# Optimization experiments

Measured on AMD Instinct MI355X. Metric: run time of the kernel, lower is better.

The kernel has to match this reference:

```python
import jax, jax.numpy as jnp
import numpy as np

E = 512
H = 8
D = E // H  # head_dim = 64
SCALE = D ** -0.5
NEG_INF = float('-inf')


def layer_norm(x, g, b, eps=1e-5):
    mu = jnp.mean(x, axis=-1, keepdims=True)
    var = jnp.var(x, axis=-1, keepdims=True)
    return (x - mu) * jax.lax.rsqrt(var + eps) * g + b


def setup_inputs() -> dict:
    key = jax.random.key(0)
    ks = jax.random.split(key, 16)
    B, Q, K = 4, 2048, 2048
    inp = {
        'query': jax.random.normal(ks[0], (B, Q, E), jnp.float32),
        'key_value': jax.random.normal(ks[1], (B, K, E), jnp.float32),
        'kv_mask': jax.random.randint(ks[2], (B, K), 0, 2) > 0,
        'sparse_mask': jax.random.randint(ks[3], (B, Q, K), 0, 2) > 0,
        'ln_q_g': jnp.ones((E,), jnp.float32),
        'ln_q_b': jnp.zeros((E,), jnp.float32),
        'ln_kv_g': jnp.ones((E,), jnp.float32),
        'ln_kv_b': jnp.zeros((E,), jnp.float32),
        # Linear weights stored as (in, out): y = x @ W + b
        'Wq': jax.random.normal(ks[4], (E, E), jnp.float32) * (E ** -0.5),
        'bq': jnp.zeros((E,), jnp.float32),
        'Wk': jax.random.normal(ks[5], (E, E), jnp.float32) * (E ** -0.5),
        'bk': jnp.zeros((E,), jnp.float32),
        'Wv': jax.random.normal(ks[6], (E, E), jnp.float32) * (E ** -0.5),
        'bv': jnp.zeros((E,), jnp.float32),
        'Wo': jax.random.normal(ks[7], (E, E), jnp.float32) * (E ** -0.5),
        'bo': jnp.zeros((E,), jnp.float32),
    }
    return inp


def reference(query, key_value, kv_mask, sparse_mask,
              ln_q_g, ln_q_b, ln_kv_g, ln_kv_b,
              Wq, bq, Wk, bk, Wv, bv, Wo, bo):
    B, Qn, _ = query.shape
    Kn = key_value.shape[1]
    qn = layer_norm(query, ln_q_g, ln_q_b)
    kvn = layer_norm(key_value, ln_kv_g, ln_kv_b)
    q = (qn @ Wq + bq).reshape(B, Qn, H, D)
    k = (kvn @ Wk + bk).reshape(B, Kn, H, D)
    v = (kvn @ Wv + bv).reshape(B, Kn, H, D)
    # scores: [B, H, Q, K]
    scores = jnp.einsum('bqhd,bkhd->bhqk', q, k) * SCALE
    mask = kv_mask[:, None, None, :] & sparse_mask[:, None, :, :]
    scores = jnp.where(mask, scores, NEG_INF)
    attn = jax.nn.softmax(scores, axis=-1)
    # nan_to_num(0): rows with no valid key -> all-zero weights
    valid_row = jnp.any(mask, axis=-1, keepdims=True)
    attn = jnp.where(valid_row, attn, 0.0)
    out = jnp.einsum('bhqk,bkhd->bqhd', attn, v).reshape(B, Qn, E)
    return out @ Wo + bo
```

## Files before the change

### kernel.cpp

```cpp
#include <hip/hip_runtime.h>
#include <hip/hip_bf16.h>
#include <math.h>

typedef unsigned short ushort_t;
typedef __attribute__((ext_vector_type(8))) __bf16 bf16x8;
typedef __attribute__((ext_vector_type(4))) float f32x4;
typedef __attribute__((ext_vector_type(16))) float f32x16;
typedef __attribute__((ext_vector_type(4))) unsigned int u32x4;

#define E_DIM 512
#define HEADS 8
#define HD 64
#define SEQ 2048
#define NROWS 8192
#define NEGF (-1e30f)
#define QSCALE 0.18033688011112042f

static __device__ __forceinline__ unsigned short f2b(float f) {
  unsigned int x;
  __builtin_memcpy(&x, &f, 4);
  x += 0x7fffu + ((x >> 16) & 1u);
  return (unsigned short)(x >> 16);
}

static __device__ __forceinline__ unsigned cvt_pk_bf16(float lo, float hi) {
  unsigned r;
  asm("v_cvt_pk_bf16_f32 %0, %1, %2" : "=v"(r) : "v"(lo), "v"(hi));
  return r;
}

static __device__ __forceinline__ float fexp2(float x) {
  float r;
  asm("v_exp_f32 %0, %1" : "=v"(r) : "v"(x));
  return r;
}

static __device__ __forceinline__ int swz(int row, int col) {
  return row * 64 + ((((col >> 3) ^ (row & 7)) & 7) << 3) + (col & 7);
}

static __device__ __forceinline__ void gl2lds16(const ushort_t* g, ushort_t* s) {
#if __has_builtin(__builtin_amdgcn_global_load_lds)
  __builtin_amdgcn_global_load_lds(
      (const __attribute__((address_space(1))) unsigned int*)(uintptr_t)g,
      (__attribute__((address_space(3))) unsigned int*)(uintptr_t)s,
      16, 0, 0);
#else
  int l = threadIdx.x & 63;
  *(u32x4*)(s + l * 8) = *(const u32x4*)g;
#endif
}

__launch_bounds__(256)
__global__ void prep_kernel(const float* __restrict__ Wq, const float* __restrict__ Wk,
                            const float* __restrict__ Wv, const float* __restrict__ Wo,
                            ushort_t* __restrict__ WT,
                            const int* __restrict__ kvm, const int* __restrict__ sp,
                            unsigned long long* __restrict__ bits,
                            const float* __restrict__ xq, const float* __restrict__ xkv,
                            const float* __restrict__ gq, const float* __restrict__ bq,
                            const float* __restrict__ gkv, const float* __restrict__ bkv,
                            ushort_t* __restrict__ yq, ushort_t* __restrict__ ykv) {
  int blk = blockIdx.x;
  int t = threadIdx.x;
  if (blk < 1024) {
    int z = blk >> 8, rem = blk & 255;
    const float* in = (z == 0) ? Wq : (z == 1) ? Wk : (z == 2) ? Wv : Wo;
    ushort_t* o = WT + (size_t)z * E_DIM * E_DIM;
    __shared__ float tile[32 * 33];
    int tx = t & 31, ty = t >> 5;
    int n0 = (rem & 15) * 32, k0 = (rem >> 4) * 32;
#pragma unroll
    for (int i = 0; i < 4; ++i) {
      int k = ty + i * 8;
      tile[k * 33 + tx] = in[(k0 + k) * E_DIM + n0 + tx];
    }
    __syncthreads();
#pragma unroll
    for (int i = 0; i < 4; ++i) {
      int n = ty + i * 8;
      o[(n0 + n) * E_DIM + k0 + tx] = f2b(tile[tx * 33 + n]);
    }
  } else if (blk < 3072) {
    int w = t >> 6, l = t & 63;
    int row = (blk - 1024) * 4 + w;
    int b = row >> 11;
    const int* sprow = sp + ((size_t)row << 11);
    const int* kvrow = kvm + (b << 11);
    unsigned long long* out = bits + ((size_t)row << 5);
#pragma unroll 4
    for (int it = 0; it < 32; ++it) {
      int k = it * 64 + l;
      unsigned long long m = __ballot(sprow[k] != 0 && kvrow[k] != 0);
      if (l == 0) out[it] = m;
    }
  } else {
    int idx = blk - 3072;
    int which = idx >> 11;
    const float* x = which ? xkv : xq;
    const float* g = which ? gkv : gq;
    const float* bb = which ? bkv : bq;
    ushort_t* y = which ? ykv : yq;
    int w = t >> 6, l = t & 63;
    int row = (idx & 2047) * 4 + w;
    f32x4 x0 = *(const f32x4*)&x[row * E_DIM + l * 8];
    f32x4 x1 = *(const f32x4*)&x[row * E_DIM + l * 8 + 4];
    float xf[8], s = 0.f, ss = 0.f;
#pragma unroll
    for (int j = 0; j < 8; ++j) {
      xf[j] = (j < 4) ? x0[j] : x1[j - 4];
      s += xf[j];
      ss += xf[j] * xf[j];
    }
#pragma unroll
    for (int off = 32; off > 0; off >>= 1) {
      s += __shfl_xor(s, off);
      ss += __shfl_xor(ss, off);
    }
    float mu = s * (1.f / 512.f);
    float var = fmaxf(ss * (1.f / 512.f) - mu * mu, 0.f);
    float rs = rsqrtf(var + 1e-5f);
    f32x4 g0 = *(const f32x4*)&g[l * 8];
    f32x4 g1 = *(const f32x4*)&g[l * 8 + 4];
    f32x4 b0 = *(const f32x4*)&bb[l * 8];
    f32x4 b1 = *(const f32x4*)&bb[l * 8 + 4];
#pragma unroll
    for (int j = 0; j < 8; ++j) {
      float gv = (j < 4) ? g0[j] : g1[j - 4];
      float bv = (j < 4) ? b0[j] : b1[j - 4];
      y[row * E_DIM + l * 8 + j] = f2b((xf[j] - mu) * rs * gv + bv);
    }
  }
}

template <int MODE>
static __device__ __forceinline__ void gemm_core64(ushort_t* lA, ushort_t* lB,
                                                   const ushort_t* __restrict__ A,
                                                   const ushort_t* __restrict__ WT,
                                                   const float* __restrict__ bias,
                                                   void* Cv, float scale, int m0, int n0) {
  int t = threadIdx.x, w = t >> 6, l = t & 63;
  int quad = l >> 4, l15 = l & 15;
  int wm_ = w >> 1, wn_ = w & 1;
  int csrc = ((l & 7) ^ (l >> 3)) * 8;
  int rln = l >> 3;

  f32x4 acc[4][2] = {};
  for (int kk = 0; kk < E_DIM; kk += 64) {
    __syncthreads();
#pragma unroll
    for (int i = 0; i < 4; ++i) {
      int r0 = i * 32 + w * 8;
      gl2lds16(&A[(size_t)(m0 + r0 + rln) * E_DIM + kk + csrc], &lA[r0 * 64]);
    }
#pragma unroll
    for (int i = 0; i < 2; ++i) {
      int r0 = i * 32 + w * 8;
      gl2lds16(&WT[(size_t)(n0 + r0 + rln) * E_DIM + kk + csrc], &lB[r0 * 64]);
    }
    __syncthreads();
#pragma unroll
    for (int ks = 0; ks < 2; ++ks) {
      bf16x8 af[4], bf[2];
#pragma unroll
      for (int mt = 0; mt < 4; ++mt)
        af[mt] = *(const bf16x8*)&lA[swz(wm_ * 64 + mt * 16 + l15, ks * 32 + quad * 8)];
#pragma unroll
      for (int nt = 0; nt < 2; ++nt)
        bf[nt] = *(const bf16x8*)&lB[swz(wn_ * 32 + nt * 16 + l15, ks * 32 + quad * 8)];
#pragma unroll
      for (int mt = 0; mt < 4; ++mt)
#pragma unroll
        for (int nt = 0; nt < 2; ++nt)
          acc[mt][nt] = __builtin_amdgcn_mfma_f32_16x16x32_bf16(af[mt], bf[nt], acc[mt][nt], 0, 0, 0);
    }
  }

#pragma unroll
  for (int nt = 0; nt < 2; ++nt) {
    int col = n0 + wn_ * 32 + nt * 16 + l15;
    float bv = bias[col];
    if constexpr (MODE == 2) {
      int h = col >> 6, d = col & 63;
#pragma unroll
      for (int mt = 0; mt < 4; ++mt) {
        int row = m0 + wm_ * 64 + mt * 16 + quad * 4;
        int b = row >> 11, k = row & 2047;
        union { ushort_t u[4]; uint2 v; } pk;
#pragma unroll
        for (int r = 0; r < 4; ++r) pk.u[r] = f2b(acc[mt][nt][r] + bv);
        *(uint2*)&((ushort_t*)Cv)[((((size_t)(b * HEADS + h)) * HD + d) << 11) + k] = pk.v;
      }
    } else {
#pragma unroll
      for (int mt = 0; mt < 4; ++mt) {
#pragma unroll
        for (int r = 0; r < 4; ++r) {
          int rowm = m0 + wm_ * 64 + mt * 16 + quad * 4 + r;
          float val = (acc[mt][nt][r] + bv) * scale;
          if constexpr (MODE == 0)
            ((ushort_t*)Cv)[rowm * E_DIM + col] = f2b(val);
          else
            ((float*)Cv)[rowm * E_DIM + col] = val;
        }
      }
    }
  }
}

__launch_bounds__(256)
__global__ void proj3_kernel(const ushort_t* __restrict__ qn, const ushort_t* __restrict__ WTq,
                             const float* __restrict__ bq, ushort_t* __restrict__ qp,
                             const ushort_t* __restrict__ kvn, const ushort_t* __restrict__ WTv,
                             const float* __restrict__ bv, ushort_t* __restrict__ Vt,
                             const ushort_t* __restrict__ WTk, const float* __restrict__ bk,
                             ushort_t* __restrict__ kp, int zbase) {
  __shared__ ushort_t lA[128 * 64];
  __shared__ ushort_t lB[64 * 64];
  int flat = blockIdx.x;
  int chunk = gridDim.x >> 3;
  int work = (flat & 7) * chunk + (flat >> 3);
  int z = zbase + (work >> 9);
  int r = work & 511;
  int m0 = (r >> 3) * 128, n0 = (r & 7) * 64;
  if (z == 0)      gemm_core64<0>(lA, lB, qn,  WTq, bq, qp, QSCALE, m0, n0);
  else if (z == 1) gemm_core64<2>(lA, lB, kvn, WTv, bv, Vt, 1.f,    m0, n0);
  else             gemm_core64<0>(lA, lB, kvn, WTk, bk, kp, 1.f,    m0, n0);
}

__launch_bounds__(256)
__global__ void out_kernel(const ushort_t* __restrict__ A, const ushort_t* __restrict__ WT,
                           const float* __restrict__ bias, float* __restrict__ C) {
  __shared__ ushort_t lA[128 * 64];
  __shared__ ushort_t lB[64 * 64];
  int flat = blockIdx.x;
  int work = (flat & 7) * 64 + (flat >> 3);
  int m0 = (work >> 3) * 128, n0 = (work & 7) * 64;
  gemm_core64<1>(lA, lB, A, WT, bias, C, 1.f, m0, n0);
}

__launch_bounds__(256)
__global__ void attn_kernel(const ushort_t* __restrict__ Qp, const ushort_t* __restrict__ Kp,
                            const ushort_t* __restrict__ Vt,
                            const unsigned long long* __restrict__ bits,
                            ushort_t* __restrict__ ctx) {
  __shared__ __align__(16) char smemb[40960];
  ushort_t* sQ = (ushort_t*)smemb;
  int t = threadIdx.x, w = t >> 6, l = t & 63;
  int qw = w & 1, ks = w >> 1;
  ushort_t* sK = (ushort_t*)(smemb + 8192 + ks * 8192);
  ushort_t* sV = (ushort_t*)(smemb + 24576 + ks * 8192);
  int l31 = l & 31, half = l >> 5;

  int flat = blockIdx.x;
  int work = (flat & 7) * 128 + (flat >> 3);
  int qblk = work & 31;
  int h = (work >> 5) & 7;
  int b = work >> 8;
  int q0 = qblk * 64;
  int bh = b * HEADS + h;
  int myq = qw * 32 + l31;
  int csrc = ((l & 7) ^ (l >> 3)) * 8;
  int rln = l >> 3;

#pragma unroll
  for (int it = 0; it < 2; ++it) {
    int r0 = w * 16 + it * 8;
    gl2lds16(&Qp[(size_t)(b * SEQ + q0 + r0 + rln) * E_DIM + h * HD + csrc], &sQ[r0 * 64]);
  }

  const unsigned long long* mrow = bits + ((size_t)(b * SEQ + q0 + myq) << 5);
  float ls0 = 0.f, ls1 = 0.f, ls2 = 0.f, ls3 = 0.f;
  f32x16 o0 = {}, o1 = {};
  bf16x8 qf[4];

  for (int t16 = 0; t16 < 16; ++t16) {
    int kt = t16 * 2 + ks;
    int k0 = kt * 64;
    unsigned long long wmask = mrow[kt];
    __syncthreads();
#pragma unroll
    for (int it = 0; it < 4; ++it) {
      int r0 = (it * 2 + qw) * 8;
      gl2lds16(&Kp[(size_t)(b * SEQ + k0 + r0 + rln) * E_DIM + h * HD + csrc], &sK[r0 * 64]);
      gl2lds16(&Vt[((size_t)bh * HD + r0 + rln) * SEQ + k0 + csrc], &sV[r0 * 64]);
    }
    __syncthreads();
    if (t16 == 0) {
#pragma unroll
      for (int ds = 0; ds < 4; ++ds)
        qf[ds] = *(const bf16x8*)&sQ[swz(myq, ds * 16 + 8 * half)];
    }

    f32x16 s0 = {}, s1 = {};
    __builtin_amdgcn_s_setprio(1);
#pragma unroll
    for (int ds = 0; ds < 4; ++ds) {
      bf16x8 kf0 = *(const bf16x8*)&sK[swz(l31, ds * 16 + 8 * half)];
      bf16x8 kf1 = *(const bf16x8*)&sK[swz(32 + l31, ds * 16 + 8 * half)];
      s0 = __builtin_amdgcn_mfma_f32_32x32x16_bf16(kf0, qf[ds], s0, 0, 0, 0);
      s1 = __builtin_amdgcn_mfma_f32_32x32x16_bf16(kf1, qf[ds], s1, 0, 0, 0);
    }
    __builtin_amdgcn_s_setprio(0);

    bf16x8 pf[4];
#pragma unroll
    for (int kt2 = 0; kt2 < 2; ++kt2) {
      const f32x16& sv = kt2 ? s1 : s0;
      unsigned h32 = ((unsigned)(wmask >> (32 * kt2))) >> (4 * half);
      unsigned wa[4], wb[4];
#pragma unroll
      for (int g = 0; g < 4; ++g) {
        unsigned gb = h32 >> (8 * g);
        float p0 = fexp2((gb & 1u)        ? sv[g * 4 + 0] : NEGF);
        float p1 = fexp2(((gb >> 1) & 1u) ? sv[g * 4 + 1] : NEGF);
        float p2 = fexp2(((gb >> 2) & 1u) ? sv[g * 4 + 2] : NEGF);
        float p3 = fexp2(((gb >> 3) & 1u) ? sv[g * 4 + 3] : NEGF);
        ls0 += p0; ls1 += p1; ls2 += p2; ls3 += p3;
        wa[g] = cvt_pk_bf16(p0, p1);
        wb[g] = cvt_pk_bf16(p2, p3);
      }
      asm("v_permlane32_swap_b32 %0, %1" : "+v"(wa[0]), "+v"(wa[1]));
      asm("v_permlane32_swap_b32 %0, %1" : "+v"(wb[0]), "+v"(wb[1]));
      asm("v_permlane32_swap_b32 %0, %1" : "+v"(wa[2]), "+v"(wa[3]));
      asm("v_permlane32_swap_b32 %0, %1" : "+v"(wb[2]), "+v"(wb[3]));
      union { unsigned u[4]; bf16x8 v; } f0, f1;
      f0.u[0] = wa[0]; f0.u[1] = wb[0]; f0.u[2] = wa[1]; f0.u[3] = wb[1];
      f1.u[0] = wa[2]; f1.u[1] = wb[2]; f1.u[2] = wa[3]; f1.u[3] = wb[3];
      pf[kt2 * 2 + 0] = f0.v;
      pf[kt2 * 2 + 1] = f1.v;
    }

    __builtin_amdgcn_s_setprio(1);
#pragma unroll
    for (int ksp = 0; ksp < 4; ++ksp) {
      bf16x8 vf0 = *(const bf16x8*)&sV[swz(l31, ksp * 16 + 8 * half)];
      bf16x8 vf1 = *(const bf16x8*)&sV[swz(32 + l31, ksp * 16 + 8 * half)];
      o0 = __builtin_amdgcn_mfma_f32_32x32x16_bf16(vf0, pf[ksp], o0, 0, 0, 0);
      o1 = __builtin_amdgcn_mfma_f32_32x32x16_bf16(vf1, pf[ksp], o1, 0, 0, 0);
    }
    __builtin_amdgcn_s_setprio(0);
  }

  float lsum = (ls0 + ls1) + (ls2 + ls3);
  lsum += __shfl_xor(lsum, 32);

  __syncthreads();
  float* mrg = (float*)(smemb + 8192);
  if (ks == 1) {
    float* e = mrg + (qw * 64 + l) * 33;
#pragma unroll
    for (int r = 0; r < 16; ++r) e[r] = o0[r];
#pragma unroll
    for (int r = 0; r < 16; ++r) e[16 + r] = o1[r];
    e[32] = lsum;
  }
  __syncthreads();
  if (ks == 0) {
    const float* e = mrg + (qw * 64 + l) * 33;
#pragma unroll
    for (int r = 0; r < 16; ++r) o0[r] += e[r];
#pragma unroll
    for (int r = 0; r < 16; ++r) o1[r] += e[16 + r];
    lsum += e[32];
    float inv = (lsum > 0.f) ? 1.f / lsum : 0.f;
    size_t base = (size_t)(b * SEQ + q0 + myq) * E_DIM + h * HD;
#pragma unroll
    for (int dt = 0; dt < 2; ++dt) {
      const f32x16& oo = dt ? o1 : o0;
#pragma unroll
      for (int g = 0; g < 4; ++g) {
        union { ushort_t u[4]; uint2 v; } ov;
#pragma unroll
        for (int r = 0; r < 4; ++r) ov.u[r] = f2b(oo[g * 4 + r] * inv);
        *(uint2*)&ctx[base + dt * 32 + g * 8 + 4 * half] = ov.v;
      }
    }
  }
}

extern "C" void kernel_launch(void* const* d_in, const int* in_sizes, int n_in,
                              void* d_out, int out_size, void* d_ws, size_t ws_size,
                              hipStream_t stream) {
  const float* query     = (const float*)d_in[0];
  const float* key_value = (const float*)d_in[1];
  const int*   kv_mask   = (const int*)d_in[2];
  const int*   sp_mask   = (const int*)d_in[3];
  const float* ln_q_g  = (const float*)d_in[4];
  const float* ln_q_b  = (const float*)d_in[5];
  const float* ln_kv_g = (const float*)d_in[6];
  const float* ln_kv_b = (const float*)d_in[7];
  const float* Wq = (const float*)d_in[8];
  const float* bq = (const float*)d_in[9];
  const float* Wk = (const float*)d_in[10];
  const float* bk = (const float*)d_in[11];
  const float* Wv = (const float*)d_in[12];
  const float* bv = (const float*)d_in[13];
  const float* Wo = (const float*)d_in[14];
  const float* bo = (const float*)d_in[15];

  const size_t NB = (size_t)NROWS * E_DIM;
  char* ws = (char*)d_ws;
  ushort_t* bufA = (ushort_t*)ws;
  ushort_t* bufB = bufA + NB;
  ushort_t* WT   = bufB + NB;
  ushort_t* WTq = WT;
  ushort_t* WTk = WTq + E_DIM * E_DIM;
  ushort_t* WTv = WTk + E_DIM * E_DIM;
  ushort_t* WTo = WTv + E_DIM * E_DIM;
  unsigned long long* bits = (unsigned long long*)(WTo + E_DIM * E_DIM);
  ushort_t* bufC = (ushort_t*)(ws + (20u << 20));

  ushort_t* dlo = (ushort_t*)d_out;
  ushort_t* dhi = dlo + NB;

  bool fused = ws_size >= (28u << 20);
  ushort_t* kp = fused ? bufC : dlo;

  prep_kernel<<<7168, 256, 0, stream>>>(Wq, Wk, Wv, Wo, WT, kv_mask, sp_mask, bits,
                                        query, key_value, ln_q_g, ln_q_b, ln_kv_g, ln_kv_b,
                                        dlo, bufA);

  if (fused) {
    proj3_kernel<<<1536, 256, 0, stream>>>(dlo, WTq, bq, dhi,
                                           bufA, WTv, bv, bufB,
                                           WTk, bk, bufC, 0);
  } else {
    proj3_kernel<<<1024, 256, 0, stream>>>(dlo, WTq, bq, dhi,
                                           bufA, WTv, bv, bufB,
                                           WTk, bk, dlo, 0);
    proj3_kernel<<<512, 256, 0, stream>>>(dlo, WTq, bq, dhi,
                                          bufA, WTv, bv, bufB,
                                          WTk, bk, dlo, 2);
  }

  attn_kernel<<<1024, 256, 0, stream>>>(dhi, kp, bufB, bits, bufA);

  out_kernel<<<512, 256, 0, stream>>>(bufA, WTo, bo, (float*)d_out);
}
```

Before: 259.6 us.

## Use 128x128 projection tiles and MFMA-based softmax row sums with bitmask masking

The QKV projection now uses 128x128 output tiles per block, half the blocks of before, with a schedule that groups the Q/K/V column blocks per row tile, so each A tile is loaded fewer times. In attention, masking is done by ANDing the exp result with a sign-extended mask bit instead of selecting before exp. The row sum is computed by an extra MFMA against a ones vector instead of scalar adds and a shuffle. This adds accumulator registers (16 acc tiles in the GEMM, an extra f32x16 in attention), which may lower occupancy.

Result: no change. 264.8 us (+2.0%).

```diff
diff --git a/kernel.cpp b/kernel.cpp
--- a/kernel.cpp
+++ b/kernel.cpp
@@ -33,6 +33,14 @@
   float r;
   asm("v_exp_f32 %0, %1" : "=v"(r) : "v"(x));
   return r;
+}
+
+static __device__ __forceinline__ unsigned bitmask1(unsigned v, int off) {
+#if __has_builtin(__builtin_amdgcn_sbfe)
+  return (unsigned)__builtin_amdgcn_sbfe((int)v, off, 1);
+#else
+  return (unsigned)((int)(v << (31 - off)) >> 31);
+#endif
 }
 
 static __device__ __forceinline__ int swz(int row, int col) {
@@ -134,6 +142,77 @@
 }
 
 template <int MODE>
+static __device__ __forceinline__ void gemm_core128(ushort_t* lA, ushort_t* lB,
+                                                    const ushort_t* __restrict__ A,
+                                                    const ushort_t* __restrict__ WT,
+                                                    const float* __restrict__ bias,
+                                                    void* Cv, float scale, int m0, int n0) {
+  int t = threadIdx.x, w = t >> 6, l = t & 63;
+  int quad = l >> 4, l15 = l & 15;
+  int wm_ = w >> 1, wn_ = w & 1;
+  int csrc = ((l & 7) ^ (l >> 3)) * 8;
+  int rln = l >> 3;
+
+  f32x4 acc[4][4] = {};
+  for (int kk = 0; kk < E_DIM; kk += 64) {
+    __syncthreads();
+#pragma unroll
+    for (int i = 0; i < 4; ++i) {
+      int r0 = i * 32 + w * 8;
+      gl2lds16(&A[(size_t)(m0 + r0 + rln) * E_DIM + kk + csrc], &lA[r0 * 64]);
+      gl2lds16(&WT[(size_t)(n0 + r0 + rln) * E_DIM + kk + csrc], &lB[r0 * 64]);
+    }
+    __syncthreads();
+#pragma unroll
+    for (int ks = 0; ks < 2; ++ks) {
+      bf16x8 af[4], bf[4];
+#pragma unroll
+      for (int mt = 0; mt < 4; ++mt)
+        af[mt] = *(const bf16x8*)&lA[swz(wm_ * 64 + mt * 16 + l15, ks * 32 + quad * 8)];
+#pragma unroll
+      for (int nt = 0; nt < 4; ++nt)
+        bf[nt] = *(const bf16x8*)&lB[swz(wn_ * 64 + nt * 16 + l15, ks * 32 + quad * 8)];
+#pragma unroll
+      for (int mt = 0; mt < 4; ++mt)
+#pragma unroll
+        for (int nt = 0; nt < 4; ++nt)
+          acc[mt][nt] = __builtin_amdgcn_mfma_f32_16x16x32_bf16(af[mt], bf[nt], acc[mt][nt], 0, 0, 0);
+    }
+  }
+
+#pragma unroll
+  for (int nt = 0; nt < 4; ++nt) {
+    int col = n0 + wn_ * 64 + nt * 16 + l15;
+    float bv = bias[col];
+    if constexpr (MODE == 2) {
+      int h = col >> 6, d = col & 63;
+#pragma unroll
+      for (int mt = 0; mt < 4; ++mt) {
+        int row = m0 + wm_ * 64 + mt * 16 + quad * 4;
+        int b = row >> 11, k = row & 2047;
+        union { ushort_t u[4]; uint2 v; } pk;
+#pragma unroll
+        for (int r = 0; r < 4; ++r) pk.u[r] = f2b(acc[mt][nt][r] + bv);
+        *(uint2*)&((ushort_t*)Cv)[((((size_t)(b * HEADS + h)) * HD + d) << 11) + k] = pk.v;
+      }
+    } else {
+#pragma unroll
+      for (int mt = 0; mt < 4; ++mt) {
+#pragma unroll
+        for (int r = 0; r < 4; ++r) {
+          int rowm = m0 + wm_ * 64 + mt * 16 + quad * 4 + r;
+          float val = (acc[mt][nt][r] + bv) * scale;
+          if constexpr (MODE == 0)
+            ((ushort_t*)Cv)[rowm * E_DIM + col] = f2b(val);
+          else
+            ((float*)Cv)[rowm * E_DIM + col] = val;
+        }
+      }
+    }
+  }
+}
+
+template <int MODE>
 static __device__ __forceinline__ void gemm_core64(ushort_t* lA, ushort_t* lB,
                                                    const ushort_t* __restrict__ A,
                                                    const ushort_t* __restrict__ WT,
@@ -180,52 +259,47 @@
   for (int nt = 0; nt < 2; ++nt) {
     int col = n0 + wn_ * 32 + nt * 16 + l15;
     float bv = bias[col];
-    if constexpr (MODE == 2) {
-      int h = col >> 6, d = col & 63;
-#pragma unroll
-      for (int mt = 0; mt < 4; ++mt) {
-        int row = m0 + wm_ * 64 + mt * 16 + quad * 4;
-        int b = row >> 11, k = row & 2047;
-        union { ushort_t u[4]; uint2 v; } pk;
-#pragma unroll
-        for (int r = 0; r < 4; ++r) pk.u[r] = f2b(acc[mt][nt][r] + bv);
-        *(uint2*)&((ushort_t*)Cv)[((((size_t)(b * HEADS + h)) * HD + d) << 11) + k] = pk.v;
+#pragma unroll
+    for (int mt = 0; mt < 4; ++mt) {
+#pragma unroll
+      for (int r = 0; r < 4; ++r) {
+        int rowm = m0 + wm_ * 64 + mt * 16 + quad * 4 + r;
+        float val = (acc[mt][nt][r] + bv) * scale;
+        if constexpr (MODE == 0)
+          ((ushort_t*)Cv)[rowm * E_DIM + col] = f2b(val);
+        else
+          ((float*)Cv)[rowm * E_DIM + col] = val;
       }
-    } else {
-#pragma unroll
-      for (int mt = 0; mt < 4; ++mt) {
-#pragma unroll
-        for (int r = 0; r < 4; ++r) {
-          int rowm = m0 + wm_ * 64 + mt * 16 + quad * 4 + r;
-          float val = (acc[mt][nt][r] + bv) * scale;
-          if constexpr (MODE == 0)
-            ((ushort_t*)Cv)[rowm * E_DIM + col] = f2b(val);
-          else
-            ((float*)Cv)[rowm * E_DIM + col] = val;
-        }
-      }
-    }
-  }
-}
-
+    }
+  }
+}
+
+template <int SCHED>
 __launch_bounds__(256)
-__global__ void proj3_kernel(const ushort_t* __restrict__ qn, const ushort_t* __restrict__ WTq,
-                             const float* __restrict__ bq, ushort_t* __restrict__ qp,
-                             const ushort_t* __restrict__ kvn, const ushort_t* __restrict__ WTv,
-                             const float* __restrict__ bv, ushort_t* __restrict__ Vt,
-                             const ushort_t* __restrict__ WTk, const float* __restrict__ bk,
-                             ushort_t* __restrict__ kp, int zbase) {
+__global__ void proj_kernel(const ushort_t* __restrict__ qn, const ushort_t* __restrict__ WTq,
+                            const float* __restrict__ bq, ushort_t* __restrict__ qp,
+                            const ushort_t* __restrict__ kvn, const ushort_t* __restrict__ WTk,
+                            const float* __restrict__ bk, ushort_t* __restrict__ kp,
+                            const ushort_t* __restrict__ WTv, const float* __restrict__ bv,
+                            ushort_t* __restrict__ Vt) {
   __shared__ ushort_t lA[128 * 64];
-  __shared__ ushort_t lB[64 * 64];
+  __shared__ ushort_t lB[128 * 64];
+  constexpr int NBN = (SCHED == 0) ? 12 : (SCHED == 1) ? 8 : 4;
   int flat = blockIdx.x;
   int chunk = gridDim.x >> 3;
   int work = (flat & 7) * chunk + (flat >> 3);
-  int z = zbase + (work >> 9);
-  int r = work & 511;
-  int m0 = (r >> 3) * 128, n0 = (r & 7) * 64;
-  if (z == 0)      gemm_core64<0>(lA, lB, qn,  WTq, bq, qp, QSCALE, m0, n0);
-  else if (z == 1) gemm_core64<2>(lA, lB, kvn, WTv, bv, Vt, 1.f,    m0, n0);
-  else             gemm_core64<0>(lA, lB, kvn, WTk, bk, kp, 1.f,    m0, n0);
+  int nb = work % NBN;
+  int m0 = (work / NBN) * 128;
+  if constexpr (SCHED == 0) {
+    if (nb < 4)      gemm_core128<0>(lA, lB, qn,  WTq, bq, qp, QSCALE, m0, nb * 128);
+    else if (nb < 8) gemm_core128<0>(lA, lB, kvn, WTk, bk, kp, 1.f,    m0, (nb - 4) * 128);
+    else             gemm_core128<2>(lA, lB, kvn, WTv, bv, Vt, 1.f,    m0, (nb - 8) * 128);
+  } else if constexpr (SCHED == 1) {
+    if (nb < 4)      gemm_core128<0>(lA, lB, qn,  WTq, bq, qp, QSCALE, m0, nb * 128);
+    else             gemm_core128<2>(lA, lB, kvn, WTv, bv, Vt, 1.f,    m0, (nb - 4) * 128);
+  } else {
+    gemm_core128<0>(lA, lB, kvn, WTk, bk, kp, 1.f, m0, nb * 128);
+  }
 }
 
 __launch_bounds__(256)
@@ -270,9 +344,11 @@
   }
 
   const unsigned long long* mrow = bits + ((size_t)(b * SEQ + q0 + myq) << 5);
-  float ls0 = 0.f, ls1 = 0.f, ls2 = 0.f, ls3 = 0.f;
-  f32x16 o0 = {}, o1 = {};
+  f32x16 o0 = {}, o1 = {}, lacc = {};
   bf16x8 qf[4];
+  union { unsigned u[4]; bf16x8 v; } onec;
+#pragma unroll
+  for (int i = 0; i < 4; ++i) onec.u[i] = 0x3f803f80u;
 
   for (int t16 = 0; t16 < 16; ++t16) {
     int kt = t16 * 2 + ks;
@@ -311,14 +387,12 @@
       unsigned wa[4], wb[4];
 #pragma unroll
       for (int g = 0; g < 4; ++g) {
-        unsigned gb = h32 >> (8 * g);
-        float p0 = fexp2((gb & 1u)        ? sv[g * 4 + 0] : NEGF);
-        float p1 = fexp2(((gb >> 1) & 1u) ? sv[g * 4 + 1] : NEGF);
-        float p2 = fexp2(((gb >> 2) & 1u) ? sv[g * 4 + 2] : NEGF);
-        float p3 = fexp2(((gb >> 3) & 1u) ? sv[g * 4 + 3] : NEGF);
-        ls0 += p0; ls1 += p1; ls2 += p2; ls3 += p3;
-        wa[g] = cvt_pk_bf16(p0, p1);
-        wb[g] = cvt_pk_bf16(p2, p3);
+        unsigned q0u = __float_as_uint(fexp2(sv[g * 4 + 0])) & bitmask1(h32, 8 * g + 0);
+        unsigned q1u = __float_as_uint(fexp2(sv[g * 4 + 1])) & bitmask1(h32, 8 * g + 1);
+        unsigned q2u = __float_as_uint(fexp2(sv[g * 4 + 2])) & bitmask1(h32, 8 * g + 2);
+        unsigned q3u = __float_as_uint(fexp2(sv[g * 4 + 3])) & bitmask1(h32, 8 * g + 3);
+        wa[g] = cvt_pk_bf16(__uint_as_float(q0u), __uint_as_float(q1u));
+        wb[g] = cvt_pk_bf16(__uint_as_float(q2u), __uint_as_float(q3u));
       }
       asm("v_permlane32_swap_b32 %0, %1" : "+v"(wa[0]), "+v"(wa[1]));
       asm("v_permlane32_swap_b32 %0, %1" : "+v"(wb[0]), "+v"(wb[1]));
@@ -338,12 +412,12 @@
       bf16x8 vf1 = *(const bf16x8*)&sV[swz(32 + l31, ksp * 16 + 8 * half)];
       o0 = __builtin_amdgcn_mfma_f32_32x32x16_bf16(vf0, pf[ksp], o0, 0, 0, 0);
       o1 = __builtin_amdgcn_mfma_f32_32x32x16_bf16(vf1, pf[ksp], o1, 0, 0, 0);
+      lacc = __builtin_amdgcn_mfma_f32_32x32x16_bf16(onec.v, pf[ksp], lacc, 0, 0, 0);
     }
     __builtin_amdgcn_s_setprio(0);
   }
 
-  float lsum = (ls0 + ls1) + (ls2 + ls3);
-  lsum += __shfl_xor(lsum, 32);
+  float lsum = lacc[0];
 
   __syncthreads();
   float* mrg = (float*)(smemb + 8192);
@@ -422,16 +496,16 @@
                                         dlo, bufA);
 
   if (fused) {
-    proj3_kernel<<<1536, 256, 0, stream>>>(dlo, WTq, bq, dhi,
-                                           bufA, WTv, bv, bufB,
-                                           WTk, bk, bufC, 0);
+    proj_kernel<0><<<768, 256, 0, stream>>>(dlo, WTq, bq, dhi,
+                                            bufA, WTk, bk, bufC,
+                                            WTv, bv, bufB);
   } else {
-    proj3_kernel<<<1024, 256, 0, stream>>>(dlo, WTq, bq, dhi,
-                                           bufA, WTv, bv, bufB,
-                                           WTk, bk, dlo, 0);
-    proj3_kernel<<<512, 256, 0, stream>>>(dlo, WTq, bq, dhi,
-                                          bufA, WTv, bv, bufB,
-                                          WTk, bk, dlo, 2);
+    proj_kernel<1><<<512, 256, 0, stream>>>(dlo, WTq, bq, dhi,
+                                            bufA, WTk, bk, dlo,
+                                            WTv, bv, bufB);
+    proj_kernel<2><<<256, 256, 0, stream>>>(dlo, WTq, bq, dhi,
+                                            bufA, WTk, bk, dlo,
+                                            WTv, bv, bufB);
   }
 
   attn_kernel<<<1024, 256, 0, stream>>>(dhi, kp, bufB, bits, bufA);
```
